# Kernel optimization log

Measured on AMD Instinct MI355X. Metric: run time of the kernel, lower is better.

## Reference

```python
import jax, jax.numpy as jnp
import numpy as np

NOISE_DIM = 32
HIDDEN_DIM = 256
DATA_DIM = 2
TEMP = 0.05
N = 16384
DIAG_PENALTY = 1e6


def _cdist(a, b):
    # Euclidean pairwise distance [Na, Nb], safe sqrt (zero grad at d==0 like torch.cdist)
    d2 = (jnp.sum(a * a, -1)[:, None] + jnp.sum(b * b, -1)[None, :]
          - 2.0 * (a @ b.T))
    d2 = jnp.maximum(d2, 0.0)
    safe = jnp.where(d2 > 0, d2, 1.0)
    return jnp.where(d2 > 0, jnp.sqrt(safe), 0.0)


def setup_inputs() -> dict:
    key = jax.random.key(0)
    ks = jax.random.split(key, 12)
    pos = jax.random.normal(ks[0], (N, DATA_DIM), dtype=jnp.float32)
    z = jax.random.normal(ks[1], (N, NOISE_DIM), dtype=jnp.float32)
    def lin(k, fan_in, fan_out):
        bound = 1.0 / np.sqrt(fan_in)
        k1, k2 = jax.random.split(k)
        W = jax.random.uniform(k1, (fan_in, fan_out), minval=-bound, maxval=bound, dtype=jnp.float32)
        b = jax.random.uniform(k2, (fan_out,), minval=-bound, maxval=bound, dtype=jnp.float32)
        return W, b
    W1, b1 = lin(ks[2], NOISE_DIM, HIDDEN_DIM)
    W2, b2 = lin(ks[3], HIDDEN_DIM, HIDDEN_DIM)
    W3, b3 = lin(ks[4], HIDDEN_DIM, HIDDEN_DIM)
    W4, b4 = lin(ks[5], HIDDEN_DIM, HIDDEN_DIM)
    W5, b5 = lin(ks[6], HIDDEN_DIM, DATA_DIM)
    return {"pos": pos, "z": z, "W1": W1, "b1": b1, "W2": W2, "b2": b2,
            "W3": W3, "b3": b3, "W4": W4, "b4": b4, "W5": W5, "b5": b5}


def reference(pos, z, W1, b1, W2, b2, W3, b3, W4, b4, W5, b5):
    # SELU MLP generator
    h = jax.nn.selu(z @ W1 + b1)
    h = jax.nn.selu(h @ W2 + b2)
    h = jax.nn.selu(h @ W3 + b3)
    h = jax.nn.selu(h @ W4 + b4)
    gen = h @ W5 + b5  # [N, D]

    y_pos = jax.lax.stop_gradient(pos)
    y_neg = jax.lax.stop_gradient(gen)

    dist_pos = _cdist(gen, y_pos)  # [N, N]
    dist_neg = _cdist(gen, y_neg)  # [N, N]
    dist_neg = dist_neg + jnp.eye(gen.shape[0], dtype=gen.dtype) * DIAG_PENALTY

    energy_pos = -TEMP * jax.nn.logsumexp(-dist_pos / TEMP, axis=1)
    energy_neg = TEMP * jax.nn.logsumexp(-dist_neg / TEMP, axis=1)
    return energy_pos + energy_neg  # [N]
```

## Files before the change

kernel.cpp:

```cpp
#include <hip/hip_runtime.h>
#include <hip/hip_bf16.h>

#define N_PTS 16384
#define TEMP_F 0.05f

typedef __attribute__((ext_vector_type(8))) short bf16x8;
typedef __attribute__((ext_vector_type(4))) float f32x4;

__device__ __forceinline__ float selu_f(float x) {
    const float scale = 1.0507009873554805f;
    const float alpha = 1.6732632423543772f;
    return x > 0.f ? scale * x : scale * alpha * (__expf(x) - 1.f);
}

__device__ __forceinline__ float fast_sqrtf(float x) {
#if __has_builtin(__builtin_amdgcn_sqrtf)
    return __builtin_amdgcn_sqrtf(x);
#else
    return sqrtf(x);
#endif
}

__device__ __forceinline__ float fast_exp2f(float x) {
#if __has_builtin(__builtin_amdgcn_exp2f)
    return __builtin_amdgcn_exp2f(x);
#else
    return exp2f(x);
#endif
}

__device__ __forceinline__ float fast_log2f(float x) {
#if __has_builtin(__builtin_amdgcn_logf)
    return __builtin_amdgcn_logf(x);
#else
    return log2f(x);
#endif
}

__device__ __forceinline__ f32x4 mfma_bf16(bf16x8 a, bf16x8 b, f32x4 c) {
    return __builtin_amdgcn_mfma_f32_16x16x32_bf16(a, b, c, 0, 0, 0);
}

__device__ __forceinline__ void split_bf16(float v, unsigned short& hi, unsigned short& lo) {
    unsigned u = __float_as_uint(v);
    hi = (unsigned short)(u >> 16);
    float ah = __uint_as_float(u & 0xFFFF0000u);
    lo = (unsigned short)(__float_as_uint(v - ah) >> 16);
}

__global__ __launch_bounds__(512) void pack_kernel(
    const float* __restrict__ W1, const float* __restrict__ W2,
    const float* __restrict__ W3, const float* __restrict__ W4,
    unsigned short* __restrict__ pk)
{
    int idx = blockIdx.x * 512 + threadIdx.x;
    if (idx >= 204800) return;
    const float* src;
    unsigned short *dh, *dl;
    int rem, kc, nt;
    if (idx < 8192) {
        src = W1; dh = pk; dl = pk + 8192;
        rem = idx;
        int g = rem >> 9;
        kc = 0; nt = g;
    } else {
        int t2 = idx - 8192;
        int ly = t2 >> 16;
        rem = t2 & 65535;
        src = (ly == 0) ? W2 : (ly == 1) ? W3 : W4;
        dh = pk + 16384 + ly * 131072;
        dl = dh + 65536;
        int g = rem >> 9;
        kc = g & 7; nt = g >> 3;
    }
    int e = rem & 7;
    int l = (rem >> 3) & 63;
    int n = nt * 16 + (l & 15);
    int k = kc * 32 + ((l >> 4) << 3) + e;
    float v = src[k * 256 + n];
    unsigned short hb, lb;
    split_bf16(v, hb, lb);
    dh[rem] = hb;
    dl[rem] = lb;
}

__global__ __launch_bounds__(512, 4) void mlp_mfma_kernel(
    const float* __restrict__ z,
    const unsigned short* __restrict__ pk,
    const float* __restrict__ b1, const float* __restrict__ b2,
    const float* __restrict__ b3, const float* __restrict__ b4,
    const float* __restrict__ W5, const float* __restrict__ b5,
    float* __restrict__ gen)
{
    __shared__ __align__(16) unsigned short Hh[64 * 256];
    __shared__ __align__(16) unsigned short Hl[64 * 256];

    const int t  = threadIdx.x;
    const int l  = t & 63;
    const int wv = t >> 6;
    const int rt = wv >> 1;
    const int ch = wv & 1;
    const int lr = l & 15;
    const int lq = l >> 4;
    const int row0 = blockIdx.x * 64;
    const int arow = rt * 16 + lr;

    {
        const float* zp = z + (row0 + arow) * 32 + lq * 8;
        f32x4 z0 = *(const f32x4*)(zp);
        f32x4 z1 = *(const f32x4*)(zp + 4);
        bf16x8 ahf, alf;
        #pragma unroll
        for (int e = 0; e < 8; e++) {
            float v = (e < 4) ? z0[e] : z1[e - 4];
            unsigned short hb, lb;
            split_bf16(v, hb, lb);
            ahf[e] = (short)hb; alf[e] = (short)lb;
        }
        const bf16x8* B1h = (const bf16x8*)(pk);
        const bf16x8* B1l = (const bf16x8*)(pk + 8192);
        f32x4 acc[8];
        #pragma unroll
        for (int tile = 0; tile < 8; tile++) {
            float bv = b1[ch * 128 + tile * 16 + lr];
            acc[tile] = (f32x4){bv, bv, bv, bv};
        }
        #pragma unroll
        for (int tile = 0; tile < 8; tile++) {
            int nt = ch * 8 + tile;
            bf16x8 bh = B1h[nt * 64 + l];
            bf16x8 bl = B1l[nt * 64 + l];
            acc[tile] = mfma_bf16(ahf, bh, acc[tile]);
            acc[tile] = mfma_bf16(ahf, bl, acc[tile]);
            acc[tile] = mfma_bf16(alf, bh, acc[tile]);
        }
        #pragma unroll
        for (int tile = 0; tile < 8; tile++) {
            #pragma unroll
            for (int r = 0; r < 4; r++) {
                float v = selu_f(acc[tile][r]);
                int rowo = rt * 16 + lq * 4 + r;
                int n = ch * 128 + tile * 16 + lr;
                int o = (2 * n) ^ ((rowo & 7) << 4);
                unsigned short hb, lb;
                split_bf16(v, hb, lb);
                Hh[rowo * 256 + (o >> 1)] = hb;
                Hl[rowo * 256 + (o >> 1)] = lb;
            }
        }
    }
    __syncthreads();

    #pragma unroll 1
    for (int ly = 0; ly < 3; ly++) {
        const unsigned short* wbase = pk + 16384 + ly * 131072;
        const bf16x8* Bh = (const bf16x8*)(wbase);
        const bf16x8* Bl = (const bf16x8*)(wbase + 65536);
        const float* bb = (ly == 0) ? b2 : (ly == 1) ? b3 : b4;
        f32x4 acc[8];
        #pragma unroll
        for (int tile = 0; tile < 8; tile++) {
            float bv = bb[ch * 128 + tile * 16 + lr];
            acc[tile] = (f32x4){bv, bv, bv, bv};
        }
        #pragma unroll 2
        for (int kc = 0; kc < 8; kc++) {
            int o = (kc * 64 + lq * 16) ^ ((arow & 7) << 4);
            bf16x8 ahf = *(const bf16x8*)(Hh + arow * 256 + (o >> 1));
            bf16x8 alf = *(const bf16x8*)(Hl + arow * 256 + (o >> 1));
            #pragma unroll
            for (int tile = 0; tile < 8; tile++) {
                int nt = ch * 8 + tile;
                bf16x8 bh = Bh[(nt * 8 + kc) * 64 + l];
                bf16x8 bl = Bl[(nt * 8 + kc) * 64 + l];
                acc[tile] = mfma_bf16(ahf, bh, acc[tile]);
                acc[tile] = mfma_bf16(ahf, bl, acc[tile]);
                acc[tile] = mfma_bf16(alf, bh, acc[tile]);
            }
        }
        __syncthreads();
        #pragma unroll
        for (int tile = 0; tile < 8; tile++) {
            #pragma unroll
            for (int r = 0; r < 4; r++) {
                float v = selu_f(acc[tile][r]);
                int rowo = rt * 16 + lq * 4 + r;
                int n = ch * 128 + tile * 16 + lr;
                int o = (2 * n) ^ ((rowo & 7) << 4);
                unsigned short hb, lb;
                split_bf16(v, hb, lb);
                Hh[rowo * 256 + (o >> 1)] = hb;
                Hl[rowo * 256 + (o >> 1)] = lb;
            }
        }
        __syncthreads();
    }

    if (t < 128) {
        int row = t & 63;
        int d = t >> 6;
        float sum = b5[d];
        #pragma unroll 4
        for (int k = 0; k < 256; k += 8) {
            int o = (2 * k) ^ ((row & 7) << 4);
            bf16x8 hh = *(const bf16x8*)(Hh + row * 256 + (o >> 1));
            bf16x8 ll = *(const bf16x8*)(Hl + row * 256 + (o >> 1));
            #pragma unroll
            for (int e = 0; e < 8; e++) {
                float hv = __uint_as_float(((unsigned)(unsigned short)hh[e]) << 16)
                         + __uint_as_float(((unsigned)(unsigned short)ll[e]) << 16);
                sum = fmaf(hv, W5[(k + e) * 2 + d], sum);
            }
        }
        gen[(row0 + row) * 2 + d] = sum;
    }
}

__global__ __launch_bounds__(1024) void mlp_kernel(
    const float* __restrict__ z,
    const float* __restrict__ W1, const float* __restrict__ b1,
    const float* __restrict__ W2, const float* __restrict__ b2,
    const float* __restrict__ W3, const float* __restrict__ b3,
    const float* __restrict__ W4, const float* __restrict__ b4,
    const float* __restrict__ W5, const float* __restrict__ b5,
    float* __restrict__ gen)
{
    __shared__ float h[256 * 64];

    const int t = threadIdx.x;
    const int r = t & 63;
    const int w = __builtin_amdgcn_readfirstlane(t >> 6);
    const int c0 = w * 16;
    const int row0 = blockIdx.x * 64;

    #pragma unroll
    for (int e = 0; e < 2; e++) {
        int f  = t + e * 1024;
        int rz = f >> 5;
        int kz = f & 31;
        h[kz * 64 + rz] = z[(row0 + rz) * 32 + kz];
    }
    __syncthreads();

    float acc[16];

    #pragma unroll
    for (int j = 0; j < 16; j++) acc[j] = b1[c0 + j];
    #pragma unroll 8
    for (int k = 0; k < 32; k++) {
        float hv = h[k * 64 + r];
        const float* Wr = W1 + k * 256 + c0;
        #pragma unroll
        for (int j = 0; j < 16; j++) acc[j] = fmaf(hv, Wr[j], acc[j]);
    }
    __syncthreads();
    #pragma unroll
    for (int j = 0; j < 16; j++) h[(c0 + j) * 64 + r] = selu_f(acc[j]);
    __syncthreads();

    for (int layer = 0; layer < 3; layer++) {
        const float* W = (layer == 0) ? W2 : (layer == 1) ? W3 : W4;
        const float* b = (layer == 0) ? b2 : (layer == 1) ? b3 : b4;
        #pragma unroll
        for (int j = 0; j < 16; j++) acc[j] = b[c0 + j];
        #pragma unroll 4
        for (int k = 0; k < 256; k++) {
            float hv = h[k * 64 + r];
            const float* Wr = W + k * 256 + c0;
            #pragma unroll
            for (int j = 0; j < 16; j++) acc[j] = fmaf(hv, Wr[j], acc[j]);
        }
        __syncthreads();
        #pragma unroll
        for (int j = 0; j < 16; j++) h[(c0 + j) * 64 + r] = selu_f(acc[j]);
        __syncthreads();
    }

    float p0 = 0.f, p1 = 0.f;
    #pragma unroll
    for (int kk = 0; kk < 16; kk++) {
        int k = c0 + kk;
        float hv = h[k * 64 + r];
        p0 = fmaf(hv, W5[k * 2 + 0], p0);
        p1 = fmaf(hv, W5[k * 2 + 1], p1);
    }
    __syncthreads();
    h[(0 * 16 + w) * 64 + r] = p0;
    h[(1 * 16 + w) * 64 + r] = p1;
    __syncthreads();
    if (t < 128) {
        int d  = t >> 6;
        int rr = t & 63;
        float sum = b5[d];
        #pragma unroll
        for (int ss = 0; ss < 16; ss++) sum += h[(d * 16 + ss) * 64 + rr];
        gen[(row0 + rr) * 2 + d] = sum;
    }
}

__global__ __launch_bounds__(512) void energy_kernel(
    const float* __restrict__ gen,
    const float* __restrict__ pos,
    float* __restrict__ out)
{
    __shared__ float4 sp[512];
    __shared__ float4 sg[512];

    const int t  = threadIdx.x;
    const int s  = t & 31;
    const int rl = t >> 5;
    const int i  = blockIdx.x * 16 + rl;
    const int diagBase = ((blockIdx.x * 16) >> 10) << 10;

    const float2 q = ((const float2*)gen)[i];

    const float cL2 = 28.853900817779268f;
    const float Tl2 = 0.034657359027997264f;
    const float cB  = 57.707801635558536f;

    float p0 = 0.f, p1 = 0.f, n0 = 0.f, n1 = 0.f;

    for (int base = 0; base < N_PTS; base += 1024) {
        __syncthreads();
        sp[t] = ((const float4*)pos)[base / 2 + t];
        sg[t] = ((const float4*)gen)[base / 2 + t];
        __syncthreads();
        if (base == diagBase) {
            #pragma unroll 4
            for (int u = 0; u < 16; u++) {
                int j = base + 2 * (s + 32 * u);
                float4 pp = sp[s + 32 * u];
                float4 gg = sg[s + 32 * u];
                float dx = q.x - pp.x, dy = q.y - pp.y;
                float d  = fast_sqrtf(fmaf(dx, dx, dy * dy));
                p0 += fast_exp2f(fmaf(-cL2, d, cB));
                dx = q.x - pp.z; dy = q.y - pp.w;
                d  = fast_sqrtf(fmaf(dx, dx, dy * dy));
                p1 += fast_exp2f(fmaf(-cL2, d, cB));
                dx = q.x - gg.x; dy = q.y - gg.y;
                d  = fast_sqrtf(fmaf(dx, dx, dy * dy));
                float e0 = fast_exp2f(fmaf(-cL2, d, cB));
                n0 += (j == i) ? 0.f : e0;
                dx = q.x - gg.z; dy = q.y - gg.w;
                d  = fast_sqrtf(fmaf(dx, dx, dy * dy));
                float e1 = fast_exp2f(fmaf(-cL2, d, cB));
                n1 += (j + 1 == i) ? 0.f : e1;
            }
        } else {
            #pragma unroll 4
            for (int u = 0; u < 16; u++) {
                float4 pp = sp[s + 32 * u];
                float4 gg = sg[s + 32 * u];
                float dx = q.x - pp.x, dy = q.y - pp.y;
                float d  = fast_sqrtf(fmaf(dx, dx, dy * dy));
                p0 += fast_exp2f(fmaf(-cL2, d, cB));
                dx = q.x - pp.z; dy = q.y - pp.w;
                d  = fast_sqrtf(fmaf(dx, dx, dy * dy));
                p1 += fast_exp2f(fmaf(-cL2, d, cB));
                dx = q.x - gg.x; dy = q.y - gg.y;
                d  = fast_sqrtf(fmaf(dx, dx, dy * dy));
                n0 += fast_exp2f(fmaf(-cL2, d, cB));
                dx = q.x - gg.z; dy = q.y - gg.w;
                d  = fast_sqrtf(fmaf(dx, dx, dy * dy));
                n1 += fast_exp2f(fmaf(-cL2, d, cB));
            }
        }
    }

    float sump = p0 + p1;
    float sumn = n0 + n1;
    #pragma unroll
    for (int m = 1; m < 32; m <<= 1) {
        sump += __shfl_xor(sump, m, 32);
        sumn += __shfl_xor(sumn, m, 32);
    }

    if (s == 0) {
        out[i] = Tl2 * (fast_log2f(sumn) - fast_log2f(sump));
    }
}

extern "C" void kernel_launch(void* const* d_in, const int* in_sizes, int n_in,
                              void* d_out, int out_size, void* d_ws, size_t ws_size,
                              hipStream_t stream) {
    const float* pos = (const float*)d_in[0];
    const float* z   = (const float*)d_in[1];
    const float* W1  = (const float*)d_in[2];
    const float* b1  = (const float*)d_in[3];
    const float* W2  = (const float*)d_in[4];
    const float* b2  = (const float*)d_in[5];
    const float* W3  = (const float*)d_in[6];
    const float* b3  = (const float*)d_in[7];
    const float* W4  = (const float*)d_in[8];
    const float* b4  = (const float*)d_in[9];
    const float* W5  = (const float*)d_in[10];
    const float* b5  = (const float*)d_in[11];

    float* gen = (float*)d_ws;
    unsigned short* pk = (unsigned short*)((char*)d_ws + 131072);
    const size_t WS_NEEDED = 131072 + (size_t)409600 * 2;

    if (ws_size >= WS_NEEDED) {
        pack_kernel<<<400, 512, 0, stream>>>(W1, W2, W3, W4, pk);
        mlp_mfma_kernel<<<N_PTS / 64, 512, 0, stream>>>(z, pk, b1, b2, b3, b4,
                                                        W5, b5, gen);
    } else {
        mlp_kernel<<<N_PTS / 64, 1024, 0, stream>>>(z, W1, b1, W2, b2, W3, b3,
                                                    W4, b4, W5, b5, gen);
    }
    energy_kernel<<<N_PTS / 16, 512, 0, stream>>>(gen, pos, (float*)d_out);
}
```

Before: 275.7 us.

## Retile MLP MFMA so each wave owns a 64x32 output strip

Each of the 8 waves in the MLP kernel now computes all 64 rows across 32 output columns (a 4x2 grid of 16x16 tiles), instead of 16 rows across 128 columns. The goal is to cut redundant global weight loads: each weight fragment is read once per block rather than by four row-tile waves. In exchange every wave reads more activation fragments from LDS, and the occupancy hint in launch bounds is dropped. The pack kernel is also rewritten to read weights coalesced by row-major k,n index and scatter into the packed layout, launched with 256-thread blocks.

Measured after the change: 235.2 us. 1.17x faster.

```diff
diff --git a/kernel.cpp b/kernel.cpp
--- a/kernel.cpp
+++ b/kernel.cpp
@@ -48,35 +48,32 @@
     lo = (unsigned short)(__float_as_uint(v - ah) >> 16);
 }
 
-__global__ __launch_bounds__(512) void pack_kernel(
+__global__ __launch_bounds__(256) void pack_kernel(
     const float* __restrict__ W1, const float* __restrict__ W2,
     const float* __restrict__ W3, const float* __restrict__ W4,
     unsigned short* __restrict__ pk)
 {
-    int idx = blockIdx.x * 512 + threadIdx.x;
+    int idx = blockIdx.x * 256 + threadIdx.x;
     if (idx >= 204800) return;
     const float* src;
     unsigned short *dh, *dl;
-    int rem, kc, nt;
+    int k, n, KC;
     if (idx < 8192) {
-        src = W1; dh = pk; dl = pk + 8192;
-        rem = idx;
-        int g = rem >> 9;
-        kc = 0; nt = g;
+        src = W1; dh = pk; dl = pk + 8192; KC = 1;
+        k = idx >> 8; n = idx & 255;
     } else {
         int t2 = idx - 8192;
         int ly = t2 >> 16;
-        rem = t2 & 65535;
+        int r2 = t2 & 65535;
         src = (ly == 0) ? W2 : (ly == 1) ? W3 : W4;
         dh = pk + 16384 + ly * 131072;
         dl = dh + 65536;
-        int g = rem >> 9;
-        kc = g & 7; nt = g >> 3;
-    }
-    int e = rem & 7;
-    int l = (rem >> 3) & 63;
-    int n = nt * 16 + (l & 15);
-    int k = kc * 32 + ((l >> 4) << 3) + e;
+        KC = 8;
+        k = r2 >> 8; n = r2 & 255;
+    }
+    int nt = n >> 4, lr = n & 15;
+    int kc = k >> 5, lq = (k >> 3) & 3, e = k & 7;
+    int rem = ((nt * KC + kc) * 64 + lq * 16 + lr) * 8 + e;
     float v = src[k * 256 + n];
     unsigned short hb, lb;
     split_bf16(v, hb, lb);
@@ -84,7 +81,7 @@
     dl[rem] = lb;
 }
 
-__global__ __launch_bounds__(512, 4) void mlp_mfma_kernel(
+__global__ __launch_bounds__(512) void mlp_mfma_kernel(
     const float* __restrict__ z,
     const unsigned short* __restrict__ pk,
     const float* __restrict__ b1, const float* __restrict__ b2,
@@ -98,54 +95,62 @@
     const int t  = threadIdx.x;
     const int l  = t & 63;
     const int wv = t >> 6;
-    const int rt = wv >> 1;
-    const int ch = wv & 1;
     const int lr = l & 15;
     const int lq = l >> 4;
     const int row0 = blockIdx.x * 64;
-    const int arow = rt * 16 + lr;
+
+    f32x4 acc[4][2];
 
     {
-        const float* zp = z + (row0 + arow) * 32 + lq * 8;
-        f32x4 z0 = *(const f32x4*)(zp);
-        f32x4 z1 = *(const f32x4*)(zp + 4);
-        bf16x8 ahf, alf;
-        #pragma unroll
-        for (int e = 0; e < 8; e++) {
-            float v = (e < 4) ? z0[e] : z1[e - 4];
-            unsigned short hb, lb;
-            split_bf16(v, hb, lb);
-            ahf[e] = (short)hb; alf[e] = (short)lb;
+        bf16x8 ah[4], al[4];
+        #pragma unroll
+        for (int m = 0; m < 4; m++) {
+            const float* zp = z + (row0 + m * 16 + lr) * 32 + lq * 8;
+            f32x4 z0 = *(const f32x4*)(zp);
+            f32x4 z1 = *(const f32x4*)(zp + 4);
+            #pragma unroll
+            for (int e = 0; e < 8; e++) {
+                float v = (e < 4) ? z0[e] : z1[e - 4];
+                unsigned short hb, lb;
+                split_bf16(v, hb, lb);
+                ah[m][e] = (short)hb; al[m][e] = (short)lb;
+            }
+        }
+        #pragma unroll
+        for (int n2 = 0; n2 < 2; n2++) {
+            float bv = b1[wv * 32 + n2 * 16 + lr];
+            #pragma unroll
+            for (int m = 0; m < 4; m++) acc[m][n2] = (f32x4){bv, bv, bv, bv};
         }
         const bf16x8* B1h = (const bf16x8*)(pk);
         const bf16x8* B1l = (const bf16x8*)(pk + 8192);
-        f32x4 acc[8];
-        #pragma unroll
-        for (int tile = 0; tile < 8; tile++) {
-            float bv = b1[ch * 128 + tile * 16 + lr];
-            acc[tile] = (f32x4){bv, bv, bv, bv};
-        }
-        #pragma unroll
-        for (int tile = 0; tile < 8; tile++) {
-            int nt = ch * 8 + tile;
+        #pragma unroll
+        for (int n2 = 0; n2 < 2; n2++) {
+            int nt = wv * 2 + n2;
             bf16x8 bh = B1h[nt * 64 + l];
             bf16x8 bl = B1l[nt * 64 + l];
-            acc[tile] = mfma_bf16(ahf, bh, acc[tile]);
-            acc[tile] = mfma_bf16(ahf, bl, acc[tile]);
-            acc[tile] = mfma_bf16(alf, bh, acc[tile]);
-        }
-        #pragma unroll
-        for (int tile = 0; tile < 8; tile++) {
-            #pragma unroll
-            for (int r = 0; r < 4; r++) {
-                float v = selu_f(acc[tile][r]);
-                int rowo = rt * 16 + lq * 4 + r;
-                int n = ch * 128 + tile * 16 + lr;
-                int o = (2 * n) ^ ((rowo & 7) << 4);
-                unsigned short hb, lb;
-                split_bf16(v, hb, lb);
-                Hh[rowo * 256 + (o >> 1)] = hb;
-                Hl[rowo * 256 + (o >> 1)] = lb;
+            #pragma unroll
+            for (int m = 0; m < 4; m++) {
+                acc[m][n2] = mfma_bf16(ah[m], bh, acc[m][n2]);
+                acc[m][n2] = mfma_bf16(ah[m], bl, acc[m][n2]);
+                acc[m][n2] = mfma_bf16(al[m], bh, acc[m][n2]);
+            }
+        }
+        #pragma unroll
+        for (int m = 0; m < 4; m++) {
+            #pragma unroll
+            for (int n2 = 0; n2 < 2; n2++) {
+                #pragma unroll
+                for (int r = 0; r < 4; r++) {
+                    float v = selu_f(acc[m][n2][r]);
+                    int rowo = m * 16 + lq * 4 + r;
+                    int n = wv * 32 + n2 * 16 + lr;
+                    int o = (2 * n) ^ ((rowo & 7) << 4);
+                    unsigned short hb, lb;
+                    split_bf16(v, hb, lb);
+                    Hh[rowo * 256 + (o >> 1)] = hb;
+                    Hl[rowo * 256 + (o >> 1)] = lb;
+                }
             }
         }
     }
@@ -157,40 +162,50 @@
         const bf16x8* Bh = (const bf16x8*)(wbase);
         const bf16x8* Bl = (const bf16x8*)(wbase + 65536);
         const float* bb = (ly == 0) ? b2 : (ly == 1) ? b3 : b4;
-        f32x4 acc[8];
-        #pragma unroll
-        for (int tile = 0; tile < 8; tile++) {
-            float bv = bb[ch * 128 + tile * 16 + lr];
-            acc[tile] = (f32x4){bv, bv, bv, bv};
-        }
-        #pragma unroll 2
+        #pragma unroll
+        for (int n2 = 0; n2 < 2; n2++) {
+            float bv = bb[wv * 32 + n2 * 16 + lr];
+            #pragma unroll
+            for (int m = 0; m < 4; m++) acc[m][n2] = (f32x4){bv, bv, bv, bv};
+        }
+        #pragma unroll 1
         for (int kc = 0; kc < 8; kc++) {
-            int o = (kc * 64 + lq * 16) ^ ((arow & 7) << 4);
-            bf16x8 ahf = *(const bf16x8*)(Hh + arow * 256 + (o >> 1));
-            bf16x8 alf = *(const bf16x8*)(Hl + arow * 256 + (o >> 1));
-            #pragma unroll
-            for (int tile = 0; tile < 8; tile++) {
-                int nt = ch * 8 + tile;
-                bf16x8 bh = Bh[(nt * 8 + kc) * 64 + l];
-                bf16x8 bl = Bl[(nt * 8 + kc) * 64 + l];
-                acc[tile] = mfma_bf16(ahf, bh, acc[tile]);
-                acc[tile] = mfma_bf16(ahf, bl, acc[tile]);
-                acc[tile] = mfma_bf16(alf, bh, acc[tile]);
-            }
-        }
-        __syncthreads();
-        #pragma unroll
-        for (int tile = 0; tile < 8; tile++) {
-            #pragma unroll
-            for (int r = 0; r < 4; r++) {
-                float v = selu_f(acc[tile][r]);
-                int rowo = rt * 16 + lq * 4 + r;
-                int n = ch * 128 + tile * 16 + lr;
-                int o = (2 * n) ^ ((rowo & 7) << 4);
-                unsigned short hb, lb;
-                split_bf16(v, hb, lb);
-                Hh[rowo * 256 + (o >> 1)] = hb;
-                Hl[rowo * 256 + (o >> 1)] = lb;
+            bf16x8 ah[4], al[4];
+            #pragma unroll
+            for (int m = 0; m < 4; m++) {
+                int arow = m * 16 + lr;
+                int o = (kc * 64 + lq * 16) ^ ((arow & 7) << 4);
+                ah[m] = *(const bf16x8*)(Hh + arow * 256 + (o >> 1));
+                al[m] = *(const bf16x8*)(Hl + arow * 256 + (o >> 1));
+            }
+            #pragma unroll
+            for (int n2 = 0; n2 < 2; n2++) {
+                bf16x8 bh = Bh[((wv * 2 + n2) * 8 + kc) * 64 + l];
+                bf16x8 bl = Bl[((wv * 2 + n2) * 8 + kc) * 64 + l];
+                #pragma unroll
+                for (int m = 0; m < 4; m++) {
+                    acc[m][n2] = mfma_bf16(ah[m], bh, acc[m][n2]);
+                    acc[m][n2] = mfma_bf16(ah[m], bl, acc[m][n2]);
+                    acc[m][n2] = mfma_bf16(al[m], bh, acc[m][n2]);
+                }
+            }
+        }
+        __syncthreads();
+        #pragma unroll
+        for (int m = 0; m < 4; m++) {
+            #pragma unroll
+            for (int n2 = 0; n2 < 2; n2++) {
+                #pragma unroll
+                for (int r = 0; r < 4; r++) {
+                    float v = selu_f(acc[m][n2][r]);
+                    int rowo = m * 16 + lq * 4 + r;
+                    int n = wv * 32 + n2 * 16 + lr;
+                    int o = (2 * n) ^ ((rowo & 7) << 4);
+                    unsigned short hb, lb;
+                    split_bf16(v, hb, lb);
+                    Hh[rowo * 256 + (o >> 1)] = hb;
+                    Hl[rowo * 256 + (o >> 1)] = lb;
+                }
             }
         }
         __syncthreads();
@@ -401,7 +416,7 @@
     const size_t WS_NEEDED = 131072 + (size_t)409600 * 2;
 
     if (ws_size >= WS_NEEDED) {
-        pack_kernel<<<400, 512, 0, stream>>>(W1, W2, W3, W4, pk);
+        pack_kernel<<<800, 256, 0, stream>>>(W1, W2, W3, W4, pk);
         mlp_mfma_kernel<<<N_PTS / 64, 512, 0, stream>>>(z, pk, b1, b2, b3, b4,
                                                         W5, b5, gen);
     } else {
```
